# Optimization experiments

Measured on AMD Instinct MI355X. Metric: run time of the kernel, lower is better.

The kernel has to match this reference:

```python
import jax, jax.numpy as jnp
import numpy as np

E = 64      # hidden_dim
FF = 128    # ff_dim
H = 4       # nhead
D = E // H  # head_dim = 16
STEPS = 16  # recursion_steps
IN = 200    # input_dim
B = 131072  # batch


def _ln(h, g, b):
    m = h.mean(-1, keepdims=True)
    v = ((h - m) ** 2).mean(-1, keepdims=True)
    return (h - m) * jax.lax.rsqrt(v + 1e-5) * g + b


def _ffn(h, w1, b1, w2, b2):
    return jax.nn.gelu(h @ w1.T + b1, approximate=False) @ w2.T + b2


def _forward(x, W_in, b_in, g_in, be_in,
             z_in_w, z_in_b, z_out_w, z_out_b,
             z_ffn_w1, z_ffn_b1, z_ffn_w2, z_ffn_b2,
             zn1_g, zn1_b, zn2_g, zn2_b,
             y_in_w, y_in_b, y_out_w, y_out_b,
             y_ffn_w1, y_ffn_b1, y_ffn_w2, y_ffn_b2,
             yn1_g, yn1_b, yn2_g, yn2_b,
             W_out, b_out):
    Bn = x.shape[0]
    x_proj = jax.nn.gelu(_ln(x @ W_in.T + b_in, g_in, be_in), approximate=False)  # [B,E]
    y0 = jnp.zeros((Bn, E), dtype=x.dtype)
    z0 = jnp.zeros((Bn, E), dtype=x.dtype)
    scale = 1.0 / np.sqrt(D).astype(np.float32)
    Wv_y = y_in_w[2 * E:]   # cross-attn over a single kv token: softmax weight == 1,
    bv_y = y_in_b[2 * E:]   # so output = out_proj(v_proj(z)) exactly (no approximation)

    def step(carry, _):
        y, z = carry
        seq = jnp.stack([x_proj, y, z], axis=1)            # [B,3,E]
        qkv = seq @ z_in_w.T + z_in_b                      # [B,3,3E]
        q, k, v = jnp.split(qkv, 3, axis=-1)
        rh = lambda t: t.reshape(Bn, 3, H, D).transpose(0, 2, 1, 3)  # [B,H,3,D]
        q, k, v = rh(q), rh(k), rh(v)
        att = jax.nn.softmax(jnp.einsum('bhsd,bhtd->bhst', q, k) * scale, axis=-1)
        o = jnp.einsum('bhst,bhtd->bhsd', att, v).transpose(0, 2, 1, 3).reshape(Bn, 3, E)
        o = o @ z_out_w.T + z_out_b
        z_res = _ln(z + o[:, 2, :], zn1_g, zn1_b)
        z2 = _ln(z_res + _ffn(z_res, z_ffn_w1, z_ffn_b1, z_ffn_w2, z_ffn_b2), zn2_g, zn2_b)
        ca = (z2 @ Wv_y.T + bv_y) @ y_out_w.T + y_out_b    # 1-token cross-attention
        y_res = _ln(y + ca, yn1_g, yn1_b)
        y2 = _ln(y_res + _ffn(y_res, y_ffn_w1, y_ffn_b1, y_ffn_w2, y_ffn_b2), yn2_g, yn2_b)
        return (y2, z2), None

    (y, z), _ = jax.lax.scan(step, (y0, z0), None, length=STEPS)
    return (y @ W_out.T + b_out)[:, 0]                     # [B]


def setup_inputs() -> dict:
    key = jax.random.key(0)
    ks = jax.random.split(key, 12)
    f = lambda k, s: jax.random.normal(k, s, dtype=jnp.float32) * 0.05
    zeros = lambda s: jnp.zeros(s, dtype=jnp.float32)
    ones = lambda s: jnp.ones(s, dtype=jnp.float32)
    return {
        'x': jax.random.normal(ks[0], (B, IN), dtype=jnp.float32),
        'W_in': f(ks[1], (E, IN)), 'b_in': zeros((E,)),
        'g_in': ones((E,)), 'be_in': zeros((E,)),
        'z_in_w': f(ks[2], (3 * E, E)), 'z_in_b': zeros((3 * E,)),
        'z_out_w': f(ks[3], (E, E)), 'z_out_b': zeros((E,)),
        'z_ffn_w1': f(ks[4], (FF, E)), 'z_ffn_b1': zeros((FF,)),
        'z_ffn_w2': f(ks[5], (E, FF)), 'z_ffn_b2': zeros((E,)),
        'zn1_g': ones((E,)), 'zn1_b': zeros((E,)),
        'zn2_g': ones((E,)), 'zn2_b': zeros((E,)),
        'y_in_w': f(ks[6], (3 * E, E)), 'y_in_b': zeros((3 * E,)),
        'y_out_w': f(ks[7], (E, E)), 'y_out_b': zeros((E,)),
        'y_ffn_w1': f(ks[8], (FF, E)), 'y_ffn_b1': zeros((FF,)),
        'y_ffn_w2': f(ks[9], (E, FF)), 'y_ffn_b2': zeros((E,)),
        'yn1_g': ones((E,)), 'yn1_b': zeros((E,)),
        'yn2_g': ones((E,)), 'yn2_b': zeros((E,)),
        'W_out': f(ks[10], (1, E)), 'b_out': zeros((1,)),
    }


def reference(x, W_in, b_in, g_in, be_in,
              z_in_w, z_in_b, z_out_w, z_out_b,
              z_ffn_w1, z_ffn_b1, z_ffn_w2, z_ffn_b2,
              zn1_g, zn1_b, zn2_g, zn2_b,
              y_in_w, y_in_b, y_out_w, y_out_b,
              y_ffn_w1, y_ffn_b1, y_ffn_w2, y_ffn_b2,
              yn1_g, yn1_b, yn2_g, yn2_b,
              W_out, b_out):
    return _forward(x, W_in, b_in, g_in, be_in,
                    z_in_w, z_in_b, z_out_w, z_out_b,
                    z_ffn_w1, z_ffn_b1, z_ffn_w2, z_ffn_b2,
                    zn1_g, zn1_b, zn2_g, zn2_b,
                    y_in_w, y_in_b, y_out_w, y_out_b,
                    y_ffn_w1, y_ffn_b1, y_ffn_w2, y_ffn_b2,
                    yn1_g, yn1_b, yn2_g, yn2_b,
                    W_out, b_out)
```

## Files before the change

### kernel.cpp

```cpp
#include <hip/hip_runtime.h>
#include <math.h>


constexpr int STEPS = 16;
constexpr int INDIM = 200;

typedef __attribute__((ext_vector_type(8))) short bfrag8;
typedef __attribute__((ext_vector_type(4))) float f32x4;
typedef __attribute__((ext_vector_type(4))) short s16x4;

constexpr int FB_WIN  = 0;
constexpr int NFRAG   = 140;
constexpr int NPARAM  = 1544;

constexpr int LB_ZQ   = 0;
constexpr int LB_ZK   = 8;
constexpr int LB_ZV   = 16;
constexpr int LB_ZOUT = 24;
constexpr int LB_ZF1  = 32;
constexpr int LB_ZF2  = 48;
constexpr int LB_YV   = 64;
constexpr int LB_YOUT = 72;
constexpr int LB_YF1  = 80;
constexpr int LB_YF2  = 96;
constexpr int NSTEADY = 112;

constexpr int PB_BIN   = 0;
constexpr int PB_GIN   = 64;
constexpr int PB_BEIN  = 128;
constexpr int PB_ZINB  = 192;
constexpr int PB_ZOUTB = 384;
constexpr int PB_ZF1B  = 448;
constexpr int PB_ZF2B  = 576;
constexpr int PB_ZN1G  = 640;
constexpr int PB_ZN1B  = 704;
constexpr int PB_ZN2G  = 768;
constexpr int PB_ZN2B  = 832;
constexpr int PB_YVB   = 896;
constexpr int PB_YOUTB = 960;
constexpr int PB_YF1B  = 1024;
constexpr int PB_YF2B  = 1152;
constexpr int PB_YN1G  = 1216;
constexpr int PB_YN1B  = 1280;
constexpr int PB_YN2G  = 1344;
constexpr int PB_YN2B  = 1408;
constexpr int PB_WOUT  = 1472;
constexpr int PB_BOUT  = 1536;

constexpr int S64      = 72;
constexpr int L_W      = 0;
constexpr int L_P      = 57344;
constexpr int L_ACT    = 60432;
constexpr int WAVE_SH  = 1152;
constexpr int NWAVE    = 16;
constexpr int ARENA_SH = L_ACT + NWAVE * WAVE_SH;

struct Params {
  const float *x, *W_in, *b_in, *g_in, *be_in;
  const float *z_in_w, *z_in_b, *z_out_w, *z_out_b;
  const float *z_ffn_w1, *z_ffn_b1, *z_ffn_w2, *z_ffn_b2;
  const float *zn1_g, *zn1_b, *zn2_g, *zn2_b;
  const float *y_in_w, *y_in_b, *y_out_w, *y_out_b;
  const float *y_ffn_w1, *y_ffn_b1, *y_ffn_w2, *y_ffn_b2;
  const float *yn1_g, *yn1_b, *yn2_g, *yn2_b;
  const float *W_out, *b_out;
  float *out;
  int nrows;
};

__device__ __forceinline__ ushort f2bf_rne(float f) {
  uint u = __float_as_uint(f);
  u += 0x7FFFu + ((u >> 16) & 1u);
  return (ushort)(u >> 16);
}

__device__ __forceinline__ ushort f2bf(float f) {
  return (ushort)((__float_as_uint(f) + 0x8000u) >> 16);
}
__device__ __forceinline__ uint pk2(float a, float b) {
  uint ua = __float_as_uint(a) + 0x8000u;
  uint ub = __float_as_uint(b) + 0x8000u;
  return (ua >> 16) | (ub & 0xFFFF0000u);
}
__device__ __forceinline__ float upk_lo(uint u) {
  return __uint_as_float(u << 16);
}
__device__ __forceinline__ float upk_hi(uint u) {
  return __uint_as_float(u & 0xFFFF0000u);
}
__device__ __forceinline__ f32x4 upk4(const uint* p) {
  f32x4 r;
  r.x = upk_lo(p[0]); r.y = upk_hi(p[0]);
  r.z = upk_lo(p[1]); r.w = upk_hi(p[1]);
  return r;
}
__device__ __forceinline__ float dot4(f32x4 a, f32x4 b) {
  return a.x * b.x + a.y * b.y + a.z * b.z + a.w * b.w;
}
__device__ __forceinline__ void stc(short* buf, int stride, int mt, int q,
                                    int s, f32x4 c) {
  s16x4 v;
  v.x = (short)f2bf(c.x); v.y = (short)f2bf(c.y);
  v.z = (short)f2bf(c.z); v.w = (short)f2bf(c.w);
  *(s16x4*)(buf + s * stride + mt * 16 + q * 4) = v;
}

__device__ __forceinline__ void c2b_p(const uint p[8], bfrag8& b0, bfrag8& b1,
                                      int lane) {
  const int srcA = (lane & 15) | ((lane & 16) << 1);
  const int srcB = srcA + 16;
  const bool odd = (lane & 32) != 0;
  uint ev0 = p[0], ev1 = p[1], ev2 = p[4], ev3 = p[5];
  uint od0 = p[2], od1 = p[3], od2 = p[6], od3 = p[7];
  uint rA0, rA1, rA2, rA3, rB0, rB1, rB2, rB3;
  {
    uint e, o;
    e = (uint)__shfl((int)ev0, srcA); o = (uint)__shfl((int)od0, srcA); rA0 = odd ? o : e;
    e = (uint)__shfl((int)ev1, srcA); o = (uint)__shfl((int)od1, srcA); rA1 = odd ? o : e;
    e = (uint)__shfl((int)ev2, srcA); o = (uint)__shfl((int)od2, srcA); rA2 = odd ? o : e;
    e = (uint)__shfl((int)ev3, srcA); o = (uint)__shfl((int)od3, srcA); rA3 = odd ? o : e;
    e = (uint)__shfl((int)ev0, srcB); o = (uint)__shfl((int)od0, srcB); rB0 = odd ? o : e;
    e = (uint)__shfl((int)ev1, srcB); o = (uint)__shfl((int)od1, srcB); rB1 = odd ? o : e;
    e = (uint)__shfl((int)ev2, srcB); o = (uint)__shfl((int)od2, srcB); rB2 = odd ? o : e;
    e = (uint)__shfl((int)ev3, srcB); o = (uint)__shfl((int)od3, srcB); rB3 = odd ? o : e;
  }
  union U { uint u[4]; bfrag8 b; };
  U u0, u1;
  u0.u[0] = rA0; u0.u[1] = rA1; u0.u[2] = rB0; u0.u[3] = rB1;
  u1.u[0] = rA2; u1.u[1] = rA3; u1.u[2] = rB2; u1.u[3] = rB3;
  b0 = u0.b; b1 = u1.b;
}
__device__ __forceinline__ void c2b(const f32x4 c[4], bfrag8& b0, bfrag8& b1,
                                    int lane) {
  uint p[8];
#pragma unroll
  for (int mt = 0; mt < 4; ++mt) {
    p[2 * mt]     = pk2(c[mt].x, c[mt].y);
    p[2 * mt + 1] = pk2(c[mt].z, c[mt].w);
  }
  c2b_p(p, b0, b1, lane);
}

template <int MT>
__device__ __forceinline__ void layerN(const short* in, const short* lw,
                                       int fbase, const float* bias, f32x4* c,
                                       int lane, int q, int s) {
  bfrag8 bf[2];
#pragma unroll
  for (int kt = 0; kt < 2; ++kt)
    bf[kt] = *(const bfrag8*)(in + s * S64 + kt * 32 + q * 8);
#pragma unroll
  for (int mt = 0; mt < MT; ++mt)
    c[mt] = *(const f32x4*)(bias + mt * 16 + q * 4);
#pragma unroll
  for (int mt = 0; mt < MT; ++mt) {
#pragma unroll
    for (int kt = 0; kt < 2; ++kt) {
      bfrag8 af = *(const bfrag8*)(lw + (fbase + mt * 2 + kt) * 512 + lane * 8);
      c[mt] = __builtin_amdgcn_mfma_f32_16x16x32_bf16(af, bf[kt], c[mt], 0, 0, 0);
    }
  }
}

template <int MT, int KT>
__device__ __forceinline__ void layerBK(const bfrag8* bf, const short* lw,
                                        int fbase, const float* bias, f32x4* c,
                                        int lane, int q) {
#pragma unroll
  for (int mt = 0; mt < MT; ++mt)
    c[mt] = *(const f32x4*)(bias + mt * 16 + q * 4);
#pragma unroll
  for (int mt = 0; mt < MT; ++mt) {
#pragma unroll
    for (int kt = 0; kt < KT; ++kt) {
      bfrag8 af = *(const bfrag8*)(lw + (fbase + mt * KT + kt) * 512 + lane * 8);
      c[mt] = __builtin_amdgcn_mfma_f32_16x16x32_bf16(af, bf[kt], c[mt], 0, 0, 0);
    }
  }
}

template <int MT>
__device__ __forceinline__ void layerB2(const bfrag8* bfA, const bfrag8* bfB,
                                        const short* lw, int fbase,
                                        const float* bias, f32x4* cA, f32x4* cB,
                                        int lane, int q) {
#pragma unroll
  for (int mt = 0; mt < MT; ++mt) {
    f32x4 b4 = *(const f32x4*)(bias + mt * 16 + q * 4);
    cA[mt] = b4; cB[mt] = b4;
  }
#pragma unroll
  for (int mt = 0; mt < MT; ++mt) {
#pragma unroll
    for (int kt = 0; kt < 2; ++kt) {
      bfrag8 af = *(const bfrag8*)(lw + (fbase + mt * 2 + kt) * 512 + lane * 8);
      cA[mt] = __builtin_amdgcn_mfma_f32_16x16x32_bf16(af, bfA[kt], cA[mt], 0, 0, 0);
      cB[mt] = __builtin_amdgcn_mfma_f32_16x16x32_bf16(af, bfB[kt], cB[mt], 0, 0, 0);
    }
  }
}

__device__ __forceinline__ void lnorm_c(f32x4 c[4], const float* g,
                                        const float* b, int q) {
  f32x4 s4 = (c[0] + c[1]) + (c[2] + c[3]);
  float sm = (s4.x + s4.y) + (s4.z + s4.w);
  sm += __shfl_xor(sm, 16); sm += __shfl_xor(sm, 32);
  float mean = sm * (1.f / 64.f);
  f32x4 vs4 = {0.f, 0.f, 0.f, 0.f};
#pragma unroll
  for (int mt = 0; mt < 4; ++mt) {
    f32x4 d = c[mt] - mean;
    c[mt] = d;
    vs4 = vs4 + d * d;
  }
  float vs = (vs4.x + vs4.y) + (vs4.z + vs4.w);
  vs += __shfl_xor(vs, 16); vs += __shfl_xor(vs, 32);
  float rs = rsqrtf(vs * (1.f / 64.f) + 1e-5f);
#pragma unroll
  for (int mt = 0; mt < 4; ++mt) {
    f32x4 g4 = *(const f32x4*)(g + mt * 16 + q * 4);
    f32x4 b4 = *(const f32x4*)(b + mt * 16 + q * 4);
    c[mt] = (c[mt] * rs) * g4 + b4;
  }
}

__device__ __forceinline__ f32x4 gelu4(f32x4 x) {
  const float K = 0.70710678118654752f;
  f32x4 ax;
  ax.x = fabsf(x.x) * K; ax.y = fabsf(x.y) * K;
  ax.z = fabsf(x.z) * K; ax.w = fabsf(x.w) * K;
  f32x4 u = ax * 0.47047f + 1.0f;
  f32x4 t;
  t.x = __builtin_amdgcn_rcpf(u.x); t.y = __builtin_amdgcn_rcpf(u.y);
  t.z = __builtin_amdgcn_rcpf(u.z); t.w = __builtin_amdgcn_rcpf(u.w);
  f32x4 poly = ((t * 0.7478556f + (-0.0958798f)) * t + 0.3480242f) * t;
  f32x4 gq = ax * ax;
  f32x4 e;
  e.x = __expf(-gq.x); e.y = __expf(-gq.y);
  e.z = __expf(-gq.z); e.w = __expf(-gq.w);
  f32x4 r = poly * e;
  f32x4 er;
  er.x = copysignf(1.0f - r.x, x.x); er.y = copysignf(1.0f - r.y, x.y);
  er.z = copysignf(1.0f - r.z, x.z); er.w = copysignf(1.0f - r.w, x.w);
  f32x4 h = x * 0.5f;
  return h + h * er;
}

__global__ void prepack_kernel(Params p, ushort* wf) {
  int f = blockIdx.x;
  int lane = threadIdx.x;

  if (f == NFRAG) {
    float* pw = (float*)(wf + (size_t)NFRAG * 512);
    for (int t = lane; t < NPARAM; t += 64) {
      float v = 0.f;
      if      (t < 64)   v = p.b_in[t];
      else if (t < 128)  v = p.g_in[t - 64];
      else if (t < 192)  v = p.be_in[t - 128];
      else if (t < 384)  v = p.z_in_b[t - 192];
      else if (t < 448)  v = p.z_out_b[t - 384];
      else if (t < 576)  v = p.z_ffn_b1[t - 448];
      else if (t < 640)  v = p.z_ffn_b2[t - 576];
      else if (t < 704)  v = p.zn1_g[t - 640];
      else if (t < 768)  v = p.zn1_b[t - 704];
      else if (t < 832)  v = p.zn2_g[t - 768];
      else if (t < 896)  v = p.zn2_b[t - 832];
      else if (t < 960)  v = p.y_in_b[128 + t - 896];
      else if (t < 1024) v = p.y_out_b[t - 960];
      else if (t < 1152) v = p.y_ffn_b1[t - 1024];
      else if (t < 1216) v = p.y_ffn_b2[t - 1152];
      else if (t < 1280) v = p.yn1_g[t - 1216];
      else if (t < 1344) v = p.yn1_b[t - 1280];
      else if (t < 1408) v = p.yn2_g[t - 1344];
      else if (t < 1472) v = p.yn2_b[t - 1408];
      else if (t < 1536) v = p.W_out[t - 1472];
      else if (t == 1536) v = p.b_out[0];
      pw[t] = v;
    }
    return;
  }

  int q = lane >> 4, r = lane & 15;
  const float* src; int K, mt, kt, l;
  if (f < 28)        { src = p.W_in;                K = 200; mt = f / 7;  kt = f % 7; }
  else if (f < 36)   { l = f - 28;  src = p.z_in_w;            K = 64;  mt = l / 2; kt = l % 2; }
  else if (f < 44)   { l = f - 36;  src = p.z_in_w + 64 * 64;  K = 64;  mt = l / 2; kt = l % 2; }
  else if (f < 52)   { l = f - 44;  src = p.z_in_w + 128 * 64; K = 64;  mt = l / 2; kt = l % 2; }
  else if (f < 60)   { l = f - 52;  src = p.z_out_w;           K = 64;  mt = l / 2; kt = l % 2; }
  else if (f < 76)   { l = f - 60;  src = p.z_ffn_w1;          K = 64;  mt = l / 2; kt = l % 2; }
  else if (f < 92)   { l = f - 76;  src = p.z_ffn_w2;          K = 128; mt = l / 4; kt = l % 4; }
  else if (f < 100)  { l = f - 92;  src = p.y_in_w + 128 * 64; K = 64;  mt = l / 2; kt = l % 2; }
  else if (f < 108)  { l = f - 100; src = p.y_out_w;           K = 64;  mt = l / 2; kt = l % 2; }
  else if (f < 124)  { l = f - 108; src = p.y_ffn_w1;          K = 64;  mt = l / 2; kt = l % 2; }
  else               { l = f - 124; src = p.y_ffn_w2;          K = 128; mt = l / 4; kt = l % 4; }

  int row = mt * 16 + r;
  int col = kt * 32 + q * 8;
  bfrag8 o;
#pragma unroll
  for (int j = 0; j < 8; ++j) {
    int cc = col + j;
    float v = (cc < K) ? src[(size_t)row * K + cc] : 0.0f;
    o[j] = (short)f2bf_rne(v);
  }
  *(bfrag8*)(wf + (size_t)f * 512 + lane * 8) = o;
}

__global__ __launch_bounds__(1024, 1)
void trm_mfma_kernel(Params p, const ushort* wf) {
  __shared__ __align__(16) short arena[ARENA_SH];
  const int tid = threadIdx.x;
  const int wave = tid >> 6, lane = tid & 63;
  const int q = lane >> 4, s = lane & 15;

  {
    const uint4* srcw = (const uint4*)(wf + (size_t)28 * 512);
    uint4* dstw = (uint4*)(arena + L_W);
    for (int i = tid; i < NSTEADY * 64; i += 1024) dstw[i] = srcw[i];
    const uint4* srcp = (const uint4*)(wf + (size_t)NFRAG * 512);
    uint4* dstp = (uint4*)(arena + L_P);
    for (int i = tid; i < NPARAM / 4; i += 1024) dstp[i] = srcp[i];
  }
  __syncthreads();

  const short* LW = arena + L_W;
  const float* P  = (const float*)(arena + L_P);
  short* TH = arena + L_ACT + wave * WAVE_SH;

  const int chunks = (p.nrows + 255) / 256;
  for (int ic = blockIdx.x; ic < chunks; ic += gridDim.x) {
    const int row0 = ic * 256 + wave * 16;
    int row = row0 + s;
    if (row >= p.nrows) row = p.nrows - 1;

    bfrag8 xpB[2];
    {
      const float* xr = p.x + (size_t)row * INDIM;
      bfrag8 xb[7];
#pragma unroll
      for (int kt = 0; kt < 7; ++kt) {
        int k0i = kt * 32 + q * 8;
        bfrag8 t;
        if (kt < 6 || q == 0) {
          f32x4 lo = *(const f32x4*)(xr + k0i);
          f32x4 hi = *(const f32x4*)(xr + k0i + 4);
          t[0] = (short)f2bf(lo.x); t[1] = (short)f2bf(lo.y);
          t[2] = (short)f2bf(lo.z); t[3] = (short)f2bf(lo.w);
          t[4] = (short)f2bf(hi.x); t[5] = (short)f2bf(hi.y);
          t[6] = (short)f2bf(hi.z); t[7] = (short)f2bf(hi.w);
        } else {
#pragma unroll
          for (int j = 0; j < 8; ++j) t[j] = 0;
        }
        xb[kt] = t;
      }
      f32x4 c[4];
#pragma unroll
      for (int mt = 0; mt < 4; ++mt)
        c[mt] = *(const f32x4*)(P + PB_BIN + mt * 16 + q * 4);
#pragma unroll
      for (int mt = 0; mt < 4; ++mt)
#pragma unroll
        for (int kt = 0; kt < 7; ++kt) {
          bfrag8 af =
              *(const bfrag8*)(wf + (size_t)(FB_WIN + mt * 7 + kt) * 512 + lane * 8);
          c[mt] = __builtin_amdgcn_mfma_f32_16x16x32_bf16(af, xb[kt], c[mt], 0, 0, 0);
        }
      lnorm_c(c, P + PB_GIN, P + PB_BEIN, q);
#pragma unroll
      for (int mt = 0; mt < 4; ++mt) c[mt] = gelu4(c[mt]);
      c2b(c, xpB[0], xpB[1], lane);
    }

    uint k0p[8], v0p[8], zCp[8], yCp[8];
    bfrag8 zB[2], yB[2];
    {
      f32x4 ck[4], cv[4];
      layerBK<4, 2>(xpB, LW, LB_ZK, P + PB_ZINB + 64, ck, lane, q);
      layerBK<4, 2>(xpB, LW, LB_ZV, P + PB_ZINB + 128, cv, lane, q);
#pragma unroll
      for (int mt = 0; mt < 4; ++mt) {
        k0p[2 * mt]     = pk2(ck[mt].x, ck[mt].y);
        k0p[2 * mt + 1] = pk2(ck[mt].z, ck[mt].w);
        v0p[2 * mt]     = pk2(cv[mt].x, cv[mt].y);
        v0p[2 * mt + 1] = pk2(cv[mt].z, cv[mt].w);
        zCp[2 * mt] = 0u; zCp[2 * mt + 1] = 0u;
        yCp[2 * mt] = 0u; yCp[2 * mt + 1] = 0u;
      }
#pragma unroll
      for (int kt = 0; kt < 2; ++kt) {
        bfrag8 t;
#pragma unroll
        for (int j = 0; j < 8; ++j) t[j] = 0;
        zB[kt] = t; yB[kt] = t;
      }
    }

    for (int st = 0; st < STEPS; ++st) {
      float w0[4], w1[4], w2[4], wi[4];
      {
        f32x4 q2[4], kz[4], ky[4];
        layerBK<4, 2>(zB, LW, LB_ZQ, P + PB_ZINB, q2, lane, q);
        layerB2<4>(zB, yB, LW, LB_ZK, P + PB_ZINB + 64, kz, ky, lane, q);
#pragma unroll
        for (int mt = 0; mt < 4; ++mt) {
          float a0 = dot4(q2[mt], upk4(k0p + 2 * mt));
          float a1 = dot4(q2[mt], ky[mt]);
          float a2 = dot4(q2[mt], kz[mt]);
          a0 += __shfl_xor(a0, 16); a0 += __shfl_xor(a0, 32);
          a1 += __shfl_xor(a1, 16); a1 += __shfl_xor(a1, 32);
          a2 += __shfl_xor(a2, 16); a2 += __shfl_xor(a2, 32);
          a0 *= 0.25f; a1 *= 0.25f; a2 *= 0.25f;
          float mx = fmaxf(a0, fmaxf(a1, a2));
          float e0 = __expf(a0 - mx), e1 = __expf(a1 - mx), e2 = __expf(a2 - mx);
          w0[mt] = e0; w1[mt] = e1; w2[mt] = e2;
          wi[mt] = __builtin_amdgcn_rcpf(e0 + e1 + e2);
        }
      }
      {
        f32x4 vz[4], vy[4];
        layerB2<4>(zB, yB, LW, LB_ZV, P + PB_ZINB + 128, vz, vy, lane, q);
#pragma unroll
        for (int mt = 0; mt < 4; ++mt) {
          f32x4 v0 = upk4(v0p + 2 * mt);
          f32x4 o = (v0 * w0[mt] + vy[mt] * w1[mt] + vz[mt] * w2[mt]) * wi[mt];
          stc(TH, S64, mt, q, s, o);
        }
      }

      uint zrp[8];
      {
        f32x4 zr[4];
        layerN<4>(TH, LW, LB_ZOUT, P + PB_ZOUTB, zr, lane, q, s);
#pragma unroll
        for (int mt = 0; mt < 4; ++mt) zr[mt] = zr[mt] + upk4(zCp + 2 * mt);
        lnorm_c(zr, P + PB_ZN1G, P + PB_ZN1B, q);
#pragma unroll
        for (int mt = 0; mt < 4; ++mt) {
          stc(TH, S64, mt, q, s, zr[mt]);
          zrp[2 * mt]     = pk2(zr[mt].x, zr[mt].y);
          zrp[2 * mt + 1] = pk2(zr[mt].z, zr[mt].w);
        }
      }

      bfrag8 hB[4];
      {
        f32x4 h8[8];
        layerN<8>(TH, LW, LB_ZF1, P + PB_ZF1B, h8, lane, q, s);
#pragma unroll
        for (int g = 0; g < 2; ++g) {
          uint ph[8];
#pragma unroll
          for (int mt = 0; mt < 4; ++mt) {
            f32x4 h = gelu4(h8[4 * g + mt]);
            ph[2 * mt]     = pk2(h.x, h.y);
            ph[2 * mt + 1] = pk2(h.z, h.w);
          }
          c2b_p(ph, hB[2 * g], hB[2 * g + 1], lane);
        }
      }
      f32x4 z2[4];
      layerBK<4, 4>(hB, LW, LB_ZF2, P + PB_ZF2B, z2, lane, q);
#pragma unroll
      for (int mt = 0; mt < 4; ++mt) z2[mt] = z2[mt] + upk4(zrp + 2 * mt);
      lnorm_c(z2, P + PB_ZN2G, P + PB_ZN2B, q);
      {
        uint zp[8];
#pragma unroll
        for (int mt = 0; mt < 4; ++mt) {
          zp[2 * mt]     = pk2(z2[mt].x, z2[mt].y);
          zp[2 * mt + 1] = pk2(z2[mt].z, z2[mt].w);
          zCp[2 * mt] = zp[2 * mt]; zCp[2 * mt + 1] = zp[2 * mt + 1];
        }
        c2b_p(zp, zB[0], zB[1], lane);
      }

      f32x4 t4[4];
      layerBK<4, 2>(zB, LW, LB_YV, P + PB_YVB, t4, lane, q);
#pragma unroll
      for (int mt = 0; mt < 4; ++mt) stc(TH, S64, mt, q, s, t4[mt]);

      uint yrp[8];
      {
        f32x4 yr[4];
        layerN<4>(TH, LW, LB_YOUT, P + PB_YOUTB, yr, lane, q, s);
#pragma unroll
        for (int mt = 0; mt < 4; ++mt) yr[mt] = yr[mt] + upk4(yCp + 2 * mt);
        lnorm_c(yr, P + PB_YN1G, P + PB_YN1B, q);
#pragma unroll
        for (int mt = 0; mt < 4; ++mt) {
          stc(TH, S64, mt, q, s, yr[mt]);
          yrp[2 * mt]     = pk2(yr[mt].x, yr[mt].y);
          yrp[2 * mt + 1] = pk2(yr[mt].z, yr[mt].w);
        }
      }

      {
        f32x4 h8[8];
        layerN<8>(TH, LW, LB_YF1, P + PB_YF1B, h8, lane, q, s);
#pragma unroll
        for (int g = 0; g < 2; ++g) {
          uint ph[8];
#pragma unroll
          for (int mt = 0; mt < 4; ++mt) {
            f32x4 h = gelu4(h8[4 * g + mt]);
            ph[2 * mt]     = pk2(h.x, h.y);
            ph[2 * mt + 1] = pk2(h.z, h.w);
          }
          c2b_p(ph, hB[2 * g], hB[2 * g + 1], lane);
        }
      }
      f32x4 y2[4];
      layerBK<4, 4>(hB, LW, LB_YF2, P + PB_YF2B, y2, lane, q);
#pragma unroll
      for (int mt = 0; mt < 4; ++mt) y2[mt] = y2[mt] + upk4(yrp + 2 * mt);
      lnorm_c(y2, P + PB_YN2G, P + PB_YN2B, q);
      {
        uint yp[8];
#pragma unroll
        for (int mt = 0; mt < 4; ++mt) {
          yp[2 * mt]     = pk2(y2[mt].x, y2[mt].y);
          yp[2 * mt + 1] = pk2(y2[mt].z, y2[mt].w);
          yCp[2 * mt] = yp[2 * mt]; yCp[2 * mt + 1] = yp[2 * mt + 1];
        }
        c2b_p(yp, yB[0], yB[1], lane);
      }
    }

    float acc = 0.f;
#pragma unroll
    for (int mt = 0; mt < 4; ++mt) {
      f32x4 w4 = *(const f32x4*)(P + PB_WOUT + mt * 16 + q * 4);
      acc += dot4(upk4(yCp + 2 * mt), w4);
    }
    acc += __shfl_xor(acc, 16); acc += __shfl_xor(acc, 32);
    if (q == 0 && (row0 + s) < p.nrows) p.out[row0 + s] = acc + P[PB_BOUT];
  }
}

extern "C" void kernel_launch(void* const* d_in, const int* in_sizes, int n_in,
                              void* d_out, int out_size, void* d_ws,
                              size_t ws_size, hipStream_t stream) {
  Params p;
  const float* const* in = (const float* const*)d_in;
  p.x        = in[0];  p.W_in     = in[1];  p.b_in     = in[2];
  p.g_in     = in[3];  p.be_in    = in[4];
  p.z_in_w   = in[5];  p.z_in_b   = in[6];
  p.z_out_w  = in[7];  p.z_out_b  = in[8];
  p.z_ffn_w1 = in[9];  p.z_ffn_b1 = in[10];
  p.z_ffn_w2 = in[11]; p.z_ffn_b2 = in[12];
  p.zn1_g    = in[13]; p.zn1_b    = in[14];
  p.zn2_g    = in[15]; p.zn2_b    = in[16];
  p.y_in_w   = in[17]; p.y_in_b   = in[18];
  p.y_out_w  = in[19]; p.y_out_b  = in[20];
  p.y_ffn_w1 = in[21]; p.y_ffn_b1 = in[22];
  p.y_ffn_w2 = in[23]; p.y_ffn_b2 = in[24];
  p.yn1_g    = in[25]; p.yn1_b    = in[26];
  p.yn2_g    = in[27]; p.yn2_b    = in[28];
  p.W_out    = in[29]; p.b_out    = in[30];
  p.out      = (float*)d_out;
  p.nrows    = in_sizes[0] / INDIM;

  if (ws_size < (size_t)NFRAG * 1024 + NPARAM * 4) return;
  ushort* wf = (ushort*)d_ws;

  hipLaunchKernelGGL(prepack_kernel, dim3(NFRAG + 1), dim3(64), 0, stream, p, wf);
  hipLaunchKernelGGL(trm_mfma_kernel, dim3(256), dim3(1024), 0, stream, p, wf);
}
```

Measured before the change: 879.5 us.

## Stream most weight fragments from global memory to fit two blocks per CU

Most steady-state weight fragments (z out-proj, z FFN, y out-proj, y FFN) are now read straight from the global prepacked buffer instead of LDS. Only the QKV and y-V fragments stay in shared memory, which shrinks LDS use enough to allow two 1024-thread blocks per CU. Launch bounds and grid size are doubled to match. The aim is higher occupancy to hide latency, at the cost of repeated global/L2 weight loads on every MFMA and tighter register limits that may cause spills.

```diff
diff --git a/kernel.cpp b/kernel.cpp
--- a/kernel.cpp
+++ b/kernel.cpp
@@ -16,14 +16,15 @@
 constexpr int LB_ZQ   = 0;
 constexpr int LB_ZK   = 8;
 constexpr int LB_ZV   = 16;
-constexpr int LB_ZOUT = 24;
-constexpr int LB_ZF1  = 32;
-constexpr int LB_ZF2  = 48;
-constexpr int LB_YV   = 64;
-constexpr int LB_YOUT = 72;
-constexpr int LB_YF1  = 80;
-constexpr int LB_YF2  = 96;
-constexpr int NSTEADY = 112;
+constexpr int LB_YV   = 24;
+constexpr int NSTEADY = 32;
+
+constexpr int GF_ZOUT = 52;
+constexpr int GF_ZF1  = 60;
+constexpr int GF_ZF2  = 76;
+constexpr int GF_YOUT = 100;
+constexpr int GF_YF1  = 108;
+constexpr int GF_YF2  = 124;
 
 constexpr int PB_BIN   = 0;
 constexpr int PB_GIN   = 64;
@@ -49,8 +50,8 @@
 
 constexpr int S64      = 72;
 constexpr int L_W      = 0;
-constexpr int L_P      = 57344;
-constexpr int L_ACT    = 60432;
+constexpr int L_P      = 16384;
+constexpr int L_ACT    = 19472;
 constexpr int WAVE_SH  = 1152;
 constexpr int NWAVE    = 16;
 constexpr int ARENA_SH = L_ACT + NWAVE * WAVE_SH;
@@ -162,6 +163,27 @@
   }
 }
 
+template <int MT>
+__device__ __forceinline__ void layerNG(const short* in, const ushort* wf,
+                                        int gbase, const float* bias, f32x4* c,
+                                        int lane, int q, int s) {
+  bfrag8 bf[2];
+#pragma unroll
+  for (int kt = 0; kt < 2; ++kt)
+    bf[kt] = *(const bfrag8*)(in + s * S64 + kt * 32 + q * 8);
+#pragma unroll
+  for (int mt = 0; mt < MT; ++mt)
+    c[mt] = *(const f32x4*)(bias + mt * 16 + q * 4);
+#pragma unroll
+  for (int mt = 0; mt < MT; ++mt) {
+#pragma unroll
+    for (int kt = 0; kt < 2; ++kt) {
+      bfrag8 af = *(const bfrag8*)(wf + (size_t)(gbase + mt * 2 + kt) * 512 + lane * 8);
+      c[mt] = __builtin_amdgcn_mfma_f32_16x16x32_bf16(af, bf[kt], c[mt], 0, 0, 0);
+    }
+  }
+}
+
 template <int MT, int KT>
 __device__ __forceinline__ void layerBK(const bfrag8* bf, const short* lw,
                                         int fbase, const float* bias, f32x4* c,
@@ -174,6 +196,23 @@
 #pragma unroll
     for (int kt = 0; kt < KT; ++kt) {
       bfrag8 af = *(const bfrag8*)(lw + (fbase + mt * KT + kt) * 512 + lane * 8);
+      c[mt] = __builtin_amdgcn_mfma_f32_16x16x32_bf16(af, bf[kt], c[mt], 0, 0, 0);
+    }
+  }
+}
+
+template <int MT, int KT>
+__device__ __forceinline__ void layerBKG(const bfrag8* bf, const ushort* wf,
+                                         int gbase, const float* bias, f32x4* c,
+                                         int lane, int q) {
+#pragma unroll
+  for (int mt = 0; mt < MT; ++mt)
+    c[mt] = *(const f32x4*)(bias + mt * 16 + q * 4);
+#pragma unroll
+  for (int mt = 0; mt < MT; ++mt) {
+#pragma unroll
+    for (int kt = 0; kt < KT; ++kt) {
+      bfrag8 af = *(const bfrag8*)(wf + (size_t)(gbase + mt * KT + kt) * 512 + lane * 8);
       c[mt] = __builtin_amdgcn_mfma_f32_16x16x32_bf16(af, bf[kt], c[mt], 0, 0, 0);
     }
   }
@@ -306,7 +345,7 @@
   *(bfrag8*)(wf + (size_t)f * 512 + lane * 8) = o;
 }
 
-__global__ __launch_bounds__(1024, 1)
+__global__ __launch_bounds__(1024, 2)
 void trm_mfma_kernel(Params p, const ushort* wf) {
   __shared__ __align__(16) short arena[ARENA_SH];
   const int tid = threadIdx.x;
@@ -316,7 +355,10 @@
   {
     const uint4* srcw = (const uint4*)(wf + (size_t)28 * 512);
     uint4* dstw = (uint4*)(arena + L_W);
-    for (int i = tid; i < NSTEADY * 64; i += 1024) dstw[i] = srcw[i];
+    for (int i = tid; i < 24 * 64; i += 1024) dstw[i] = srcw[i];
+    const uint4* srcy = (const uint4*)(wf + (size_t)92 * 512);
+    uint4* dsty = (uint4*)(arena + L_W + 24 * 512);
+    for (int i = tid; i < 8 * 64; i += 1024) dsty[i] = srcy[i];
     const uint4* srcp = (const uint4*)(wf + (size_t)NFRAG * 512);
     uint4* dstp = (uint4*)(arena + L_P);
     for (int i = tid; i < NPARAM / 4; i += 1024) dstp[i] = srcp[i];
@@ -431,7 +473,7 @@
       uint zrp[8];
       {
         f32x4 zr[4];
-        layerN<4>(TH, LW, LB_ZOUT, P + PB_ZOUTB, zr, lane, q, s);
+        layerNG<4>(TH, wf, GF_ZOUT, P + PB_ZOUTB, zr, lane, q, s);
 #pragma unroll
         for (int mt = 0; mt < 4; ++mt) zr[mt] = zr[mt] + upk4(zCp + 2 * mt);
         lnorm_c(zr, P + PB_ZN1G, P + PB_ZN1B, q);
@@ -446,7 +488,7 @@
       bfrag8 hB[4];
       {
         f32x4 h8[8];
-        layerN<8>(TH, LW, LB_ZF1, P + PB_ZF1B, h8, lane, q, s);
+        layerNG<8>(TH, wf, GF_ZF1, P + PB_ZF1B, h8, lane, q, s);
 #pragma unroll
         for (int g = 0; g < 2; ++g) {
           uint ph[8];
@@ -460,7 +502,7 @@
         }
       }
       f32x4 z2[4];
-      layerBK<4, 4>(hB, LW, LB_ZF2, P + PB_ZF2B, z2, lane, q);
+      layerBKG<4, 4>(hB, wf, GF_ZF2, P + PB_ZF2B, z2, lane, q);
 #pragma unroll
       for (int mt = 0; mt < 4; ++mt) z2[mt] = z2[mt] + upk4(zrp + 2 * mt);
       lnorm_c(z2, P + PB_ZN2G, P + PB_ZN2B, q);
@@ -483,7 +525,7 @@
       uint yrp[8];
       {
         f32x4 yr[4];
-        layerN<4>(TH, LW, LB_YOUT, P + PB_YOUTB, yr, lane, q, s);
+        layerNG<4>(TH, wf, GF_YOUT, P + PB_YOUTB, yr, lane, q, s);
 #pragma unroll
         for (int mt = 0; mt < 4; ++mt) yr[mt] = yr[mt] + upk4(yCp + 2 * mt);
         lnorm_c(yr, P + PB_YN1G, P + PB_YN1B, q);
@@ -497,7 +539,7 @@
 
       {
         f32x4 h8[8];
-        layerN<8>(TH, LW, LB_YF1, P + PB_YF1B, h8, lane, q, s);
+        layerNG<8>(TH, wf, GF_YF1, P + PB_YF1B, h8, lane, q, s);
 #pragma unroll
         for (int g = 0; g < 2; ++g) {
           uint ph[8];
@@ -511,7 +553,7 @@
         }
       }
       f32x4 y2[4];
-      layerBK<4, 4>(hB, LW, LB_YF2, P + PB_YF2B, y2, lane, q);
+      layerBKG<4, 4>(hB, wf, GF_YF2, P + PB_YF2B, y2, lane, q);
 #pragma unroll
       for (int mt = 0; mt < 4; ++mt) y2[mt] = y2[mt] + upk4(yrp + 2 * mt);
       lnorm_c(y2, P + PB_YN2G, P + PB_YN2B, q);
@@ -565,5 +607,5 @@
   ushort* wf = (ushort*)d_ws;
 
   hipLaunchKernelGGL(prepack_kernel, dim3(NFRAG + 1), dim3(64), 0, stream, p, wf);
-  hipLaunchKernelGGL(trm_mfma_kernel, dim3(256), dim3(1024), 0, stream, p, wf);
-}
+  hipLaunchKernelGGL(trm_mfma_kernel, dim3(512), dim3(1024), 0, stream, p, wf);
+}
```

Measured after the change: 2.355 ms. +167.8%, slower.
